# Kernel tuning notes

Hardware: AMD Instinct MI355X
Metric: run time of the kernel (lower is better)

The kernel has to match this reference:

```python
import jax, jax.numpy as jnp
import numpy as np

V, D, H, L, F, S, B = 32000, 1024, 16, 6, 4096, 2048, 2
HD = D // H
EPS = 1e-5


def _pos_encoding(seq_len, d_model):
    pos = jnp.arange(seq_len, dtype=jnp.float32)[:, None]
    div = jnp.exp(jnp.arange(0, d_model, 2, dtype=jnp.float32) * (-np.log(10000.0) / d_model))
    pe = jnp.zeros((seq_len, d_model), dtype=jnp.float32)
    pe = pe.at[:, 0::2].set(jnp.sin(pos * div))
    pe = pe.at[:, 1::2].set(jnp.cos(pos * div))
    return pe


def setup_inputs() -> dict:
    key = jax.random.key(0)
    ks = jax.random.split(key, 16)
    tokens = jax.random.randint(ks[0], (B, S), 0, V, dtype=jnp.int64)
    mask = jnp.ones((B, 1, 1, S), dtype=jnp.int32)
    emb = jax.random.normal(ks[1], (V, D), dtype=jnp.float32) * 0.02
    sa = 1.0 / np.sqrt(D)
    sf = 1.0 / np.sqrt(F)
    return {
        "tokens": tokens,
        "mask": mask,
        "emb": emb,
        "Wq": jax.random.normal(ks[2], (L, D, D), dtype=jnp.float32) * sa,
        "bq": jnp.zeros((L, D), dtype=jnp.float32),
        "Wk": jax.random.normal(ks[3], (L, D, D), dtype=jnp.float32) * sa,
        "bk": jnp.zeros((L, D), dtype=jnp.float32),
        "Wv": jax.random.normal(ks[4], (L, D, D), dtype=jnp.float32) * sa,
        "bv": jnp.zeros((L, D), dtype=jnp.float32),
        "Wo": jax.random.normal(ks[5], (L, D, D), dtype=jnp.float32) * sa,
        "bo": jnp.zeros((L, D), dtype=jnp.float32),
        "W1": jax.random.normal(ks[6], (L, D, F), dtype=jnp.float32) * sa,
        "b1": jnp.zeros((L, F), dtype=jnp.float32),
        "W2": jax.random.normal(ks[7], (L, F, D), dtype=jnp.float32) * sf,
        "b2": jnp.zeros((L, D), dtype=jnp.float32),
        "g1": jnp.ones((L, D), dtype=jnp.float32),
        "be1": jnp.zeros((L, D), dtype=jnp.float32),
        "g2": jnp.ones((L, D), dtype=jnp.float32),
        "be2": jnp.zeros((L, D), dtype=jnp.float32),
    }


def _layer_norm(x, g, b):
    m = jnp.mean(x, axis=-1, keepdims=True)
    v = jnp.mean(jnp.square(x - m), axis=-1, keepdims=True)
    return (x - m) * jax.lax.rsqrt(v + EPS) * g + b


def _encoder_stack(x, mask, params):
    scale = 1.0 / np.sqrt(HD)

    def layer(x, p):
        Wq, bq, Wk, bk, Wv, bv, Wo, bo, W1, b1, W2, b2, g1, be1, g2, be2 = p
        b, s, d = x.shape
        q = (x @ Wq + bq).reshape(b, s, H, HD).transpose(0, 2, 1, 3)  # [B,H,S,HD]
        k = (x @ Wk + bk).reshape(b, s, H, HD).transpose(0, 2, 1, 3)
        v = (x @ Wv + bv).reshape(b, s, H, HD).transpose(0, 2, 1, 3)
        scores = jnp.einsum("bhqd,bhkd->bhqk", q, k) * scale
        scores = jnp.where(mask == 0, -1e9, scores)
        attn = jax.nn.softmax(scores, axis=-1)
        ctx = jnp.einsum("bhqk,bhkd->bhqd", attn, v)
        attn_out = ctx.transpose(0, 2, 1, 3).reshape(b, s, d) @ Wo + bo
        x = _layer_norm(x + attn_out, g1, be1)
        ff = jax.nn.relu(x @ W1 + b1) @ W2 + b2
        x = _layer_norm(x + ff, g2, be2)
        return x, None

    x, _ = jax.lax.scan(layer, x, params)
    return x


def reference(tokens, mask, emb, Wq, bq, Wk, bk, Wv, bv, Wo, bo, W1, b1, W2, b2, g1, be1, g2, be2):
    x = emb[tokens] + _pos_encoding(tokens.shape[1], emb.shape[1])[None]
    params = (Wq, bq, Wk, bk, Wv, bv, Wo, bo, W1, b1, W2, b2, g1, be1, g2, be2)
    return _encoder_stack(x, mask, params)
```

## Files before the change

### kernel.cpp

```cpp
#include <hip/hip_runtime.h>
#include <hip/hip_bf16.h>
#include <cstdint>
#include <cstddef>


typedef __bf16 bf16;
typedef __bf16 bf16x2 __attribute__((ext_vector_type(2)));
typedef __bf16 bf16x4 __attribute__((ext_vector_type(4)));
typedef __bf16 bf16x8 __attribute__((ext_vector_type(8)));
typedef float  f32x4  __attribute__((ext_vector_type(4)));

#define MFMA16(a, b, c) __builtin_amdgcn_mfma_f32_16x16x32_bf16((a), (b), (c), 0, 0, 0)

static __device__ __forceinline__ void load_lds16(const void* g, void* l) {
  __builtin_amdgcn_global_load_lds((const __attribute__((address_space(1))) void*)g,
                                   (__attribute__((address_space(3))) void*)l, 16, 0, 0);
}

#define BAR()   __builtin_amdgcn_s_barrier()
#define SCH0()  __builtin_amdgcn_sched_barrier(0)
#define VMCNT8() asm volatile("s_waitcnt vmcnt(8)" ::: "memory")
#define VMCNT0() asm volatile("s_waitcnt vmcnt(0)" ::: "memory")

__global__ __launch_bounds__(256) void embed_kernel(const int* __restrict__ tok,
                                                    const float* __restrict__ emb,
                                                    bf16* __restrict__ xo) {
  const int row = blockIdx.x;
  const int s = row & 2047;
  const int t = tok[row];
  const int d0 = threadIdx.x * 4;
  const float4 e = *(const float4*)&emb[(size_t)t * 1024 + d0];
  const float* ef = (const float*)&e;
  bf16x4 o4;
#pragma unroll
  for (int j = 0; j < 4; ++j) {
    const int d = d0 + j;
    const float div = __expf(-(float)(d & ~1) * 0.00899447301950864f);
    const float arg = (float)s * div;
    const float pe = (d & 1) ? cosf(arg) : sinf(arg);
    o4[j] = (bf16)(ef[j] + pe);
  }
  *(bf16x4*)&xo[(size_t)row * 1024 + d0] = o4;
}

struct TJob { const float* src; bf16* dst; int K; int N; int t0; };
struct TArgs { TJob j[6]; };

__global__ __launch_bounds__(256) void wtrans_kernel(TArgs a) {
  __shared__ float t[32][33];
  const int blk = blockIdx.x;
  const float* src = a.j[0].src; bf16* dst = a.j[0].dst;
  int K = a.j[0].K, N = a.j[0].N, t0 = a.j[0].t0;
#pragma unroll
  for (int q = 1; q < 6; ++q)
    if (blk >= a.j[q].t0) { src = a.j[q].src; dst = a.j[q].dst; K = a.j[q].K; N = a.j[q].N; t0 = a.j[q].t0; }
  const int tj = blk - t0;
  const int tilesK = K >> 5;
  const int tk = (tj % tilesK) << 5;
  const int tn = (tj / tilesK) << 5;
  const int lx = threadIdx.x & 31, ly = threadIdx.x >> 5;
#pragma unroll
  for (int i = 0; i < 4; ++i)
    t[ly + 8 * i][lx] = src[(size_t)(tk + ly + 8 * i) * N + tn + lx];
  __syncthreads();
#pragma unroll
  for (int i = 0; i < 4; ++i)
    dst[(size_t)(tn + ly + 8 * i) * K + tk + lx] = (bf16)t[lx][ly + 8 * i];
}

__global__ __launch_bounds__(256) void vtrans_kernel(const bf16* __restrict__ v,
                                                     bf16* __restrict__ vt) {
  __shared__ bf16 t[64][72];
  const int bh = blockIdx.y;
  const int s0 = blockIdx.x * 64;
  const int tid = threadIdx.x;
#pragma unroll
  for (int it = 0; it < 2; ++it) {
    const int idx = tid + it * 256;
    const int sr = idx >> 3, h8 = (idx & 7) * 8;
    *(bf16x8*)&t[sr][h8] = *(const bf16x8*)&v[((size_t)bh * 2048 + s0 + sr) * 64 + h8];
  }
  __syncthreads();
#pragma unroll
  for (int it = 0; it < 2; ++it) {
    const int idx = tid + it * 256;
    const int hd = idx >> 3, s8 = (idx & 7) * 8;
    bf16x8 o;
#pragma unroll
    for (int j = 0; j < 8; ++j) o[j] = t[s8 + j][hd];
    *(bf16x8*)&vt[((size_t)bh * 64 + hd) * 2048 + s0 + s8] = o;
  }
}

static __device__ __forceinline__ bf16x8 ldsfrag(const bf16* base, int row, int colb) {
  int off = row * 128 + colb;
  off ^= ((off >> 7) & 7) << 4;
  return *(const bf16x8*)((const char*)base + off);
}

static __device__ __forceinline__ void stage_tile(const bf16* __restrict__ Ag,
    const bf16* __restrict__ Bg, int Kstr, int kt, bf16* lA, bf16* lB, int tid) {
  const char* wbaseA = (const char*)lA + ((tid >> 6) << 10);
  const char* wbaseB = (const char*)lB + ((tid >> 6) << 10);
#pragma unroll
  for (int s = 0; s < 4; ++s) {
    const int L = s * 8192 + tid * 16;
    const int off = L ^ (((L >> 7) & 7) << 4);
    load_lds16(Ag + (size_t)(off >> 7) * Kstr + kt * 64 + ((off & 127) >> 1),
               (void*)(wbaseA + s * 8192));
  }
#pragma unroll
  for (int s = 0; s < 4; ++s) {
    const int L = s * 8192 + tid * 16;
    const int off = L ^ (((L >> 7) & 7) << 4);
    load_lds16(Bg + (size_t)(off >> 7) * Kstr + kt * 64 + ((off & 127) >> 1),
               (void*)(wbaseB + s * 8192));
  }
}

static __device__ __forceinline__ void compute_tile(const bf16* lA, const bf16* lB,
    int wm, int wn, int lr, int lg, f32x4 (&acc)[8][4]) {
  bf16x8 bfr[4][2];
#pragma unroll
  for (int n = 0; n < 4; ++n)
#pragma unroll
    for (int kk = 0; kk < 2; ++kk)
      bfr[n][kk] = ldsfrag(lB, wn * 64 + n * 16 + lr, kk * 64 + lg * 16);
#pragma unroll
  for (int m = 0; m < 8; ++m) {
    const bf16x8 a0 = ldsfrag(lA, wm * 128 + m * 16 + lr, lg * 16);
    const bf16x8 a1 = ldsfrag(lA, wm * 128 + m * 16 + lr, 64 + lg * 16);
    __builtin_amdgcn_s_setprio(1);
#pragma unroll
    for (int n = 0; n < 4; ++n) {
      acc[m][n] = MFMA16(a0, bfr[n][0], acc[m][n]);
      acc[m][n] = MFMA16(a1, bfr[n][1], acc[m][n]);
    }
    __builtin_amdgcn_s_setprio(0);
  }
}

template <int EPI>
__global__ __launch_bounds__(512, 2) void gemm256(
    const bf16* __restrict__ A, const bf16* __restrict__ Bt,
    int Kstr, int Kloop, int Nn, int nbx,
    const float* __restrict__ bias0, const float* __restrict__ bias1,
    const float* __restrict__ bias2, bf16* __restrict__ outb,
    float* __restrict__ pout,
    bf16* __restrict__ q_out, bf16* __restrict__ k_out, bf16* __restrict__ v_out) {
  __shared__ __align__(16) bf16 lds[4][16384];
  const int bz = blockIdx.y;
  const bf16* Abase = A + (size_t)bz * Kloop;
  const bf16* Bbase = Bt + (size_t)bz * Kloop;
  const int cpx = gridDim.x >> 3;
  const int wg = (blockIdx.x & 7) * cpx + (blockIdx.x >> 3);
  const int bx = wg % nbx, by = wg / nbx;
  const int tid = threadIdx.x;
  const int lane = tid & 63, wave = tid >> 6;
  const int lr = lane & 15, lg = lane >> 4;
  const int wm = wave >> 2, wn = wave & 3;
  const int m0 = by * 256, n0 = bx * 256;

  const bf16* Ag = Abase + (size_t)m0 * Kstr;
  const bf16* Bg = Bbase + (size_t)n0 * Kstr;
  bf16* LA0 = lds[0]; bf16* LB0 = lds[1];
  bf16* LA1 = lds[2]; bf16* LB1 = lds[3];

  f32x4 acc[8][4] = {};
  const int T = Kloop >> 6;

  stage_tile(Ag, Bg, Kstr, 0, LA0, LB0, tid);
  stage_tile(Ag, Bg, Kstr, 1, LA1, LB1, tid);
  VMCNT8(); BAR(); SCH0();

  for (int t = 0; t + 3 < T; t += 2) {
    compute_tile(LA0, LB0, wm, wn, lr, lg, acc);
    BAR(); SCH0();
    stage_tile(Ag, Bg, Kstr, t + 2, LA0, LB0, tid);
    VMCNT8(); BAR(); SCH0();
    compute_tile(LA1, LB1, wm, wn, lr, lg, acc);
    BAR(); SCH0();
    stage_tile(Ag, Bg, Kstr, t + 3, LA1, LB1, tid);
    VMCNT8(); BAR(); SCH0();
  }
  compute_tile(LA0, LB0, wm, wn, lr, lg, acc);
  VMCNT0(); BAR(); SCH0();
  compute_tile(LA1, LB1, wm, wn, lr, lg, acc);

#pragma unroll
  for (int m = 0; m < 8; ++m)
#pragma unroll
    for (int n = 0; n < 4; ++n)
#pragma unroll
      for (int r = 0; r < 4; ++r) {
        const int row = m0 + wm * 128 + m * 16 + lg * 4 + r;
        const int col = n0 + wn * 64 + n * 16 + lr;
        float val = acc[m][n][r];
        if (EPI == 0) {
          const int which = col >> 10, hc = col & 1023;
          const float* bs = (which == 0) ? bias0 : (which == 1) ? bias1 : bias2;
          bf16* dst = (which == 0) ? q_out : (which == 1) ? k_out : v_out;
          val += bs[hc];
          const int b = row >> 11, s = row & 2047;
          const int h = hc >> 6, hd = hc & 63;
          dst[(((size_t)b * 16 + h) * 2048 + s) * 64 + hd] = (bf16)val;
        } else if (EPI == 1) {
          pout[(size_t)bz * 4096 * 1024 + (size_t)row * 1024 + col] = val;
        } else {
          val += bias0[col];
          outb[(size_t)row * Nn + col] = (bf16)(val > 0.f ? val : 0.f);
        }
      }
}

__global__ __launch_bounds__(256) void gemm_sk(
    const bf16* __restrict__ A, const bf16* __restrict__ Bt,
    int Kstride, int Kloop, int nbx, float* __restrict__ pout) {
  __shared__ __align__(16) bf16 As[128 * 32];
  __shared__ __align__(16) bf16 Bs[128 * 32];
  const int bz = blockIdx.y;
  const bf16* Ab = A + (size_t)bz * Kloop;
  const bf16* Bb = Bt + (size_t)bz * Kloop;
  float* pb = pout + (size_t)bz * 4096 * 1024;
  const int cpx = gridDim.x >> 3;
  const int wg = (blockIdx.x & 7) * cpx + (blockIdx.x >> 3);
  const int bx = wg % nbx, by = wg / nbx;
  const int tid = threadIdx.x;
  const int lane = tid & 63;
  const int wave = tid >> 6;
  const int lr = lane & 15, lg = lane >> 4;
  const int m0 = by * 128;
  const int n0 = bx * 128;
  const int wr = (wave >> 1) * 64, wc = (wave & 1) * 64;

  f32x4 acc[4][4] = {};

  const int idx0 = tid, idx1 = tid + 256;
  const char* gA0 = (const char*)(Ab + (size_t)(m0 + (idx0 >> 2)) * Kstride) + (idx0 & 3) * 16;
  const char* gA1 = (const char*)(Ab + (size_t)(m0 + (idx1 >> 2)) * Kstride) + (idx1 & 3) * 16;
  const char* gB0 = (const char*)(Bb + (size_t)(n0 + (idx0 >> 2)) * Kstride) + (idx0 & 3) * 16;
  const char* gB1 = (const char*)(Bb + (size_t)(n0 + (idx1 >> 2)) * Kstride) + (idx1 & 3) * 16;
  bf16* lA0 = &As[(wave * 64) * 8];
  bf16* lA1 = &As[(256 + wave * 64) * 8];
  bf16* lB0 = &Bs[(wave * 64) * 8];
  bf16* lB1 = &Bs[(256 + wave * 64) * 8];

  const int ksteps = Kloop >> 5;
  for (int kt = 0; kt < ksteps; ++kt) {
    load_lds16(gA0, lA0); load_lds16(gA1, lA1);
    load_lds16(gB0, lB0); load_lds16(gB1, lB1);
    gA0 += 64; gA1 += 64; gB0 += 64; gB1 += 64;
    __syncthreads();
    bf16x8 af[2], bfr[2];
    bf16x8 af2[2], bfr2[2];
#pragma unroll
    for (int i = 0; i < 4; ++i) {
      bf16x8 a = *(const bf16x8*)&As[(wr + i * 16 + lr) * 32 + lg * 8];
      if (i < 2) af[i] = a; else af2[i - 2] = a;
    }
#pragma unroll
    for (int j = 0; j < 4; ++j) {
      bf16x8 b = *(const bf16x8*)&Bs[(wc + j * 16 + lr) * 32 + lg * 8];
      if (j < 2) bfr[j] = b; else bfr2[j - 2] = b;
    }
#pragma unroll
    for (int i = 0; i < 4; ++i)
#pragma unroll
      for (int j = 0; j < 4; ++j) {
        const bf16x8 a = (i < 2) ? af[i & 1] : af2[i & 1];
        const bf16x8 b = (j < 2) ? bfr[j & 1] : bfr2[j & 1];
        acc[i][j] = MFMA16(a, b, acc[i][j]);
      }
    __syncthreads();
  }

#pragma unroll
  for (int i = 0; i < 4; ++i)
#pragma unroll
    for (int j = 0; j < 4; ++j)
#pragma unroll
      for (int r = 0; r < 4; ++r) {
        const int row = m0 + wr + i * 16 + lg * 4 + r;
        const int col = n0 + wc + j * 16 + lr;
        pb[(size_t)row * 1024 + col] = acc[i][j][r];
      }
}

__global__ __launch_bounds__(256) void attn_kernel(const bf16* __restrict__ q,
                                                   const bf16* __restrict__ k,
                                                   const bf16* __restrict__ vt,
                                                   bf16* __restrict__ ctxo) {
  __shared__ __align__(16) bf16 Kl[64][64];
  __shared__ __align__(16) bf16 Vt[64][64];
  __shared__ __align__(16) bf16 Pl[4][16][64];
  const int tid = threadIdx.x;
  const int lane = tid & 63, w = tid >> 6;
  const int lr = lane & 15, lg = lane >> 4;
  const int swz = lr & 7;
  const int bh = blockIdx.y;
  const int q0 = blockIdx.x * 64;

  const bf16* qp = q + ((size_t)bh * 2048 + q0 + w * 16) * 64;
  bf16x8 qf0 = *(const bf16x8*)&qp[lr * 64 + lg * 8];
  bf16x8 qf1 = *(const bf16x8*)&qp[lr * 64 + lg * 8 + 32];
  const float qs = 0.18033688011112042f;
#pragma unroll
  for (int j = 0; j < 8; ++j) {
    qf0[j] = (bf16)((float)qf0[j] * qs);
    qf1[j] = (bf16)((float)qf1[j] * qs);
  }
  bf16x8 ones8;
#pragma unroll
  for (int j = 0; j < 8; ++j) ones8[j] = (bf16)1.0f;

  const bf16* kbase = k + (size_t)bh * 2048 * 64;
  const bf16* vtb = vt + (size_t)bh * 64 * 2048;

  const int sr0 = tid >> 3, sr1 = sr0 + 32;
  const int c0 = (tid & 7) * 8;
  const int cs0 = c0 ^ ((sr0 & 7) << 3);
  const int cs1 = c0 ^ ((sr1 & 7) << 3);

  f32x4 acc[4] = {};
  f32x4 accl = {};
  float mq = -1e30f;

  bf16x8 kr[2][2], vr[2][2];
  kr[0][0] = *(const bf16x8*)&kbase[(size_t)sr0 * 64 + c0];
  kr[0][1] = *(const bf16x8*)&kbase[(size_t)sr1 * 64 + c0];
  vr[0][0] = *(const bf16x8*)&vtb[(size_t)sr0 * 2048 + c0];
  vr[0][1] = *(const bf16x8*)&vtb[(size_t)sr1 * 2048 + c0];

#pragma unroll 2
  for (int c = 0; c < 32; ++c) {
    const int pp = c & 1;
    *(bf16x8*)&Kl[sr0][cs0] = kr[pp][0];
    *(bf16x8*)&Kl[sr1][cs1] = kr[pp][1];
    *(bf16x8*)&Vt[sr0][cs0] = vr[pp][0];
    *(bf16x8*)&Vt[sr1][cs1] = vr[pp][1];
    if (c + 1 < 32) {
      const int key0n = (c + 1) * 64;
      kr[pp ^ 1][0] = *(const bf16x8*)&kbase[(size_t)(key0n + sr0) * 64 + c0];
      kr[pp ^ 1][1] = *(const bf16x8*)&kbase[(size_t)(key0n + sr1) * 64 + c0];
      vr[pp ^ 1][0] = *(const bf16x8*)&vtb[(size_t)sr0 * 2048 + key0n + c0];
      vr[pp ^ 1][1] = *(const bf16x8*)&vtb[(size_t)sr1 * 2048 + key0n + c0];
    }
    __syncthreads();

    f32x4 st[4];
    __builtin_amdgcn_s_setprio(1);
#pragma unroll
    for (int ks = 0; ks < 4; ++ks) {
      const bf16x8 kf0 = *(const bf16x8*)&Kl[ks * 16 + lr][(lg ^ swz) << 3];
      const bf16x8 kf1 = *(const bf16x8*)&Kl[ks * 16 + lr][((lg + 4) ^ swz) << 3];
      f32x4 sa = {};
      sa = MFMA16(kf0, qf0, sa);
      sa = MFMA16(kf1, qf1, sa);
      st[ks] = sa;
    }
    __builtin_amdgcn_s_setprio(0);

    float mk[4];
#pragma unroll
    for (int ks = 0; ks < 4; ++ks)
      mk[ks] = fmaxf(fmaxf(st[ks][0], st[ks][1]), fmaxf(st[ks][2], st[ks][3]));
    float mx = fmaxf(fmaxf(mk[0], mk[1]), fmaxf(mk[2], mk[3]));
    mx = fmaxf(mx, __shfl_xor(mx, 16));
    mx = fmaxf(mx, __shfl_xor(mx, 32));
    if (!__all(mx - mq <= 8.0f)) {
      const float resc = exp2f(mq - mx);
      mq = mx;
      float rq[4];
#pragma unroll
      for (int r = 0; r < 4; ++r) rq[r] = __shfl(resc, lg * 4 + r);
#pragma unroll
      for (int r = 0; r < 4; ++r) {
        accl[r] *= rq[r];
#pragma unroll
        for (int jn = 0; jn < 4; ++jn) acc[jn][r] *= rq[r];
      }
    }
#pragma unroll
    for (int ks = 0; ks < 4; ++ks) {
      bf16x4 pk;
#pragma unroll
      for (int r = 0; r < 4; ++r) pk[r] = (bf16)exp2f(st[ks][r] - mq);
      const int col = (((ks * 2 + (lg >> 1)) ^ swz) << 3) + ((lg & 1) << 2);
      *(bf16x4*)&Pl[w][lr][col] = pk;
    }

    const bf16x8 pf0 = *(const bf16x8*)&Pl[w][lr][(lg ^ swz) << 3];
    const bf16x8 pf1 = *(const bf16x8*)&Pl[w][lr][((lg + 4) ^ swz) << 3];
    __builtin_amdgcn_s_setprio(1);
#pragma unroll
    for (int jn = 0; jn < 4; ++jn) {
      const bf16x8 vf0 = *(const bf16x8*)&Vt[jn * 16 + lr][(lg ^ swz) << 3];
      const bf16x8 vf1 = *(const bf16x8*)&Vt[jn * 16 + lr][((lg + 4) ^ swz) << 3];
      acc[jn] = MFMA16(pf0, vf0, acc[jn]);
      acc[jn] = MFMA16(pf1, vf1, acc[jn]);
    }
    accl = MFMA16(pf0, ones8, accl);
    accl = MFMA16(pf1, ones8, accl);
    __builtin_amdgcn_s_setprio(0);
    __syncthreads();
  }

  const int bb = bh >> 4, hh = bh & 15;
#pragma unroll
  for (int r = 0; r < 4; ++r) {
    const float inv = 1.f / accl[r];
    const size_t rowg = (size_t)bb * 2048 + q0 + w * 16 + lg * 4 + r;
#pragma unroll
    for (int jn = 0; jn < 4; ++jn)
      ctxo[rowg * 1024 + hh * 64 + jn * 16 + lr] = (bf16)(acc[jn][r] * inv);
  }
}

template <int NP>
__global__ __launch_bounds__(256) void ln2_kernel(const float* __restrict__ p,
                                                  const bf16* __restrict__ resid,
                                                  const float* __restrict__ bias,
                                                  const float* __restrict__ g,
                                                  const float* __restrict__ be,
                                                  bf16* __restrict__ xo) {
  const int row = blockIdx.x, tid = threadIdx.x;
  const bf16x4 rv = *(const bf16x4*)&resid[(size_t)row * 1024 + tid * 4];
  const float4 bb = ((const float4*)bias)[tid];
  float4 v;
  v.x = bb.x + (float)rv[0];
  v.y = bb.y + (float)rv[1];
  v.z = bb.z + (float)rv[2];
  v.w = bb.w + (float)rv[3];
#pragma unroll
  for (int pl = 0; pl < NP; ++pl) {
    const float4 a = ((const float4*)(p + (size_t)pl * 4096 * 1024 + (size_t)row * 1024))[tid];
    v.x += a.x; v.y += a.y; v.z += a.z; v.w += a.w;
  }
  float s = v.x + v.y + v.z + v.w;
  float s2 = v.x * v.x + v.y * v.y + v.z * v.z + v.w * v.w;
#pragma unroll
  for (int o = 32; o > 0; o >>= 1) { s += __shfl_down(s, o); s2 += __shfl_down(s2, o); }
  __shared__ float red[8];
  if ((tid & 63) == 0) { red[tid >> 6] = s; red[4 + (tid >> 6)] = s2; }
  __syncthreads();
  s = red[0] + red[1] + red[2] + red[3];
  s2 = red[4] + red[5] + red[6] + red[7];
  const float mean = s * (1.f / 1024.f);
  const float var = s2 * (1.f / 1024.f) - mean * mean;
  const float rstd = rsqrtf(var + 1e-5f);
  const float4 gv = ((const float4*)g)[tid];
  const float4 bv = ((const float4*)be)[tid];
  bf16x4 o4;
  o4[0] = (bf16)((v.x - mean) * rstd * gv.x + bv.x);
  o4[1] = (bf16)((v.y - mean) * rstd * gv.y + bv.y);
  o4[2] = (bf16)((v.z - mean) * rstd * gv.z + bv.z);
  o4[3] = (bf16)((v.w - mean) * rstd * gv.w + bv.w);
  *(bf16x4*)&xo[(size_t)row * 1024 + tid * 4] = o4;
}

__global__ __launch_bounds__(256) void to_f32_kernel(const bf16* __restrict__ x,
                                                     float* __restrict__ o) {
  const size_t i = ((size_t)blockIdx.x * 256 + threadIdx.x) * 4;
  const bf16x4 v = *(const bf16x4*)&x[i];
  float4 f;
  f.x = (float)v[0]; f.y = (float)v[1]; f.z = (float)v[2]; f.w = (float)v[3];
  *(float4*)&o[i] = f;
}

extern "C" void kernel_launch(void* const* d_in, const int* in_sizes, int n_in,
                              void* d_out, int out_size, void* d_ws, size_t ws_size,
                              hipStream_t stream) {
  const int* tokens = (const int*)d_in[0];
  const float* emb = (const float*)d_in[2];
  const float* Wq = (const float*)d_in[3];
  const float* bq = (const float*)d_in[4];
  const float* Wk = (const float*)d_in[5];
  const float* bk = (const float*)d_in[6];
  const float* Wv = (const float*)d_in[7];
  const float* bv = (const float*)d_in[8];
  const float* Wo = (const float*)d_in[9];
  const float* bo = (const float*)d_in[10];
  const float* W1 = (const float*)d_in[11];
  const float* b1 = (const float*)d_in[12];
  const float* W2 = (const float*)d_in[13];
  const float* b2 = (const float*)d_in[14];
  const float* g1 = (const float*)d_in[15];
  const float* be1 = (const float*)d_in[16];
  const float* g2 = (const float*)d_in[17];
  const float* be2 = (const float*)d_in[18];

  char* p = (char*)d_ws;
  auto carve = [&](size_t bytes) { char* r = p; p += (bytes + 255) & ~(size_t)255; return r; };
  bf16* wt_qkv = (bf16*)carve((size_t)3072 * 1024 * 2);
  bf16* wt_o   = (bf16*)carve((size_t)1024 * 1024 * 2);
  bf16* wt_1   = (bf16*)carve((size_t)4096 * 1024 * 2);
  bf16* wt_2   = (bf16*)carve((size_t)1024 * 4096 * 2);
  bf16* xb     = (bf16*)carve((size_t)4096 * 1024 * 2);
  bf16* qb     = (bf16*)carve((size_t)4096 * 1024 * 2);
  bf16* kb     = (bf16*)carve((size_t)4096 * 1024 * 2);
  bf16* vb     = (bf16*)carve((size_t)4096 * 1024 * 2);
  bf16* vtb    = (bf16*)carve((size_t)4096 * 1024 * 2);
  bf16* ctxb   = (bf16*)carve((size_t)4096 * 1024 * 2);
  float* pb    = (float*)carve((size_t)4 * 4096 * 1024 * 4);
  bf16* hb     = (bf16*)carve((size_t)4096 * 4096 * 2);

  embed_kernel<<<4096, 256, 0, stream>>>(tokens, emb, xb);

  for (int l = 0; l < 6; ++l) {
    TArgs ta;
    ta.j[0] = { Wq + (size_t)l * 1024 * 1024, wt_qkv,                  1024, 1024, 0 };
    ta.j[1] = { Wk + (size_t)l * 1024 * 1024, wt_qkv + 1024 * 1024,    1024, 1024, 1024 };
    ta.j[2] = { Wv + (size_t)l * 1024 * 1024, wt_qkv + 2 * 1024 * 1024,1024, 1024, 2048 };
    ta.j[3] = { Wo + (size_t)l * 1024 * 1024, wt_o,                    1024, 1024, 3072 };
    ta.j[4] = { W1 + (size_t)l * 1024 * 4096, wt_1,                    1024, 4096, 4096 };
    ta.j[5] = { W2 + (size_t)l * 4096 * 1024, wt_2,                    4096, 1024, 8192 };
    wtrans_kernel<<<12288, 256, 0, stream>>>(ta);

    gemm256<0><<<192, 512, 0, stream>>>(xb, wt_qkv, 1024, 1024, 3072, 12,
        bq + (size_t)l * 1024, bk + (size_t)l * 1024, bv + (size_t)l * 1024,
        nullptr, nullptr, qb, kb, vb);

    vtrans_kernel<<<dim3(32, 32), 256, 0, stream>>>(vb, vtb);

    attn_kernel<<<dim3(32, 32), 256, 0, stream>>>(qb, kb, vtb, ctxb);

    gemm_sk<<<dim3(256, 2), 256, 0, stream>>>(ctxb, wt_o, 1024, 512, 8, pb);
    ln2_kernel<2><<<4096, 256, 0, stream>>>(pb, xb, bo + (size_t)l * 1024,
        g1 + (size_t)l * 1024, be1 + (size_t)l * 1024, xb);

    gemm256<2><<<256, 512, 0, stream>>>(xb, wt_1, 1024, 1024, 4096, 16,
        b1 + (size_t)l * 4096, nullptr, nullptr, hb,
        nullptr, nullptr, nullptr, nullptr);

    gemm256<1><<<dim3(64, 4), 512, 0, stream>>>(hb, wt_2, 4096, 1024, 1024, 4,
        nullptr, nullptr, nullptr, nullptr, pb,
        nullptr, nullptr, nullptr);
    ln2_kernel<4><<<4096, 256, 0, stream>>>(pb, xb, b2 + (size_t)l * 1024,
        g2 + (size_t)l * 1024, be2 + (size_t)l * 1024, xb);
  }

  to_f32_kernel<<<4096, 256, 0, stream>>>(xb, (float*)d_out);
}
```

Before: 1.517 ms.

## Double-buffer attention K/V tiles in LDS with direct global-to-LDS loads

Replaces the register-staged K/V prefetch in the attention kernel with global_load_lds transfers into two LDS buffers per operand. Loads for the tile two steps ahead are issued right after the current buffer has been consumed, and vmcnt waits plus barriers keep producer and consumer in step. This is meant to cut the VGPR staging and ds_write instructions and to overlap memory latency with MFMA work. In exchange it doubles the K/V LDS footprint, which may lower occupancy, and it relies on a swizzled source-address computation and manual wait counts being exactly right.

```diff
diff --git a/kernel.cpp b/kernel.cpp
--- a/kernel.cpp
+++ b/kernel.cpp
@@ -20,6 +20,7 @@
 #define BAR()   __builtin_amdgcn_s_barrier()
 #define SCH0()  __builtin_amdgcn_sched_barrier(0)
 #define VMCNT8() asm volatile("s_waitcnt vmcnt(8)" ::: "memory")
+#define VMCNT4() asm volatile("s_waitcnt vmcnt(4)" ::: "memory")
 #define VMCNT0() asm volatile("s_waitcnt vmcnt(0)" ::: "memory")
 
 __global__ __launch_bounds__(256) void embed_kernel(const int* __restrict__ tok,
@@ -290,8 +291,8 @@
                                                    const bf16* __restrict__ k,
                                                    const bf16* __restrict__ vt,
                                                    bf16* __restrict__ ctxo) {
-  __shared__ __align__(16) bf16 Kl[64][64];
-  __shared__ __align__(16) bf16 Vt[64][64];
+  __shared__ __align__(16) bf16 Kl[2][4096];
+  __shared__ __align__(16) bf16 Vl[2][4096];
   __shared__ __align__(16) bf16 Pl[4][16][64];
   const int tid = threadIdx.x;
   const int lane = tid & 63, w = tid >> 6;
@@ -315,44 +316,33 @@
 
   const bf16* kbase = k + (size_t)bh * 2048 * 64;
   const bf16* vtb = vt + (size_t)bh * 64 * 2048;
-
-  const int sr0 = tid >> 3, sr1 = sr0 + 32;
-  const int c0 = (tid & 7) * 8;
-  const int cs0 = c0 ^ ((sr0 & 7) << 3);
-  const int cs1 = c0 ^ ((sr1 & 7) << 3);
+  const int wb = w << 10;
 
   f32x4 acc[4] = {};
   f32x4 accl = {};
   float mq = -1e30f;
 
-  bf16x8 kr[2][2], vr[2][2];
-  kr[0][0] = *(const bf16x8*)&kbase[(size_t)sr0 * 64 + c0];
-  kr[0][1] = *(const bf16x8*)&kbase[(size_t)sr1 * 64 + c0];
-  vr[0][0] = *(const bf16x8*)&vtb[(size_t)sr0 * 2048 + c0];
-  vr[0][1] = *(const bf16x8*)&vtb[(size_t)sr1 * 2048 + c0];
-
-#pragma unroll 2
-  for (int c = 0; c < 32; ++c) {
-    const int pp = c & 1;
-    *(bf16x8*)&Kl[sr0][cs0] = kr[pp][0];
-    *(bf16x8*)&Kl[sr1][cs1] = kr[pp][1];
-    *(bf16x8*)&Vt[sr0][cs0] = vr[pp][0];
-    *(bf16x8*)&Vt[sr1][cs1] = vr[pp][1];
-    if (c + 1 < 32) {
-      const int key0n = (c + 1) * 64;
-      kr[pp ^ 1][0] = *(const bf16x8*)&kbase[(size_t)(key0n + sr0) * 64 + c0];
-      kr[pp ^ 1][1] = *(const bf16x8*)&kbase[(size_t)(key0n + sr1) * 64 + c0];
-      vr[pp ^ 1][0] = *(const bf16x8*)&vtb[(size_t)sr0 * 2048 + key0n + c0];
-      vr[pp ^ 1][1] = *(const bf16x8*)&vtb[(size_t)sr1 * 2048 + key0n + c0];
-    }
-    __syncthreads();
-
+  auto stage = [&](int c, bf16* dK, bf16* dV) {
+    const bf16* gK = kbase + (size_t)c * 64 * 64;
+    const bf16* gV = vtb + c * 64;
+#pragma unroll
+    for (int s = 0; s < 2; ++s) {
+      const int L = s * 4096 + tid * 16;
+      const int off = L ^ (((L >> 7) & 7) << 4);
+      load_lds16(gK + (size_t)(off >> 7) * 64 + ((off & 127) >> 1),
+                 (char*)dK + s * 4096 + wb);
+      load_lds16(gV + (size_t)(off >> 7) * 2048 + ((off & 127) >> 1),
+                 (char*)dV + s * 4096 + wb);
+    }
+  };
+
+  auto body = [&](const bf16* Kb, const bf16* Vb) {
     f32x4 st[4];
     __builtin_amdgcn_s_setprio(1);
 #pragma unroll
     for (int ks = 0; ks < 4; ++ks) {
-      const bf16x8 kf0 = *(const bf16x8*)&Kl[ks * 16 + lr][(lg ^ swz) << 3];
-      const bf16x8 kf1 = *(const bf16x8*)&Kl[ks * 16 + lr][((lg + 4) ^ swz) << 3];
+      const bf16x8 kf0 = *(const bf16x8*)&Kb[(ks * 16 + lr) * 64 + ((lg ^ swz) << 3)];
+      const bf16x8 kf1 = *(const bf16x8*)&Kb[(ks * 16 + lr) * 64 + (((lg + 4) ^ swz) << 3)];
       f32x4 sa = {};
       sa = MFMA16(kf0, qf0, sa);
       sa = MFMA16(kf1, qf1, sa);
@@ -394,16 +384,33 @@
     __builtin_amdgcn_s_setprio(1);
 #pragma unroll
     for (int jn = 0; jn < 4; ++jn) {
-      const bf16x8 vf0 = *(const bf16x8*)&Vt[jn * 16 + lr][(lg ^ swz) << 3];
-      const bf16x8 vf1 = *(const bf16x8*)&Vt[jn * 16 + lr][((lg + 4) ^ swz) << 3];
+      const bf16x8 vf0 = *(const bf16x8*)&Vb[(jn * 16 + lr) * 64 + ((lg ^ swz) << 3)];
+      const bf16x8 vf1 = *(const bf16x8*)&Vb[(jn * 16 + lr) * 64 + (((lg + 4) ^ swz) << 3)];
       acc[jn] = MFMA16(pf0, vf0, acc[jn]);
       acc[jn] = MFMA16(pf1, vf1, acc[jn]);
     }
     accl = MFMA16(pf0, ones8, accl);
     accl = MFMA16(pf1, ones8, accl);
     __builtin_amdgcn_s_setprio(0);
-    __syncthreads();
-  }
+  };
+
+  stage(0, Kl[0], Vl[0]);
+  stage(1, Kl[1], Vl[1]);
+  VMCNT4(); BAR(); SCH0();
+
+  for (int c = 0; c + 3 < 32; c += 2) {
+    body(Kl[0], Vl[0]);
+    BAR(); SCH0();
+    stage(c + 2, Kl[0], Vl[0]);
+    VMCNT4(); BAR(); SCH0();
+    body(Kl[1], Vl[1]);
+    BAR(); SCH0();
+    stage(c + 3, Kl[1], Vl[1]);
+    VMCNT4(); BAR(); SCH0();
+  }
+  body(Kl[0], Vl[0]);
+  VMCNT0(); BAR(); SCH0();
+  body(Kl[1], Vl[1]);
 
   const int bb = bh >> 4, hh = bh & 15;
 #pragma unroll
```

Measured after the change: 1.545 ms. No clear change (+1.8%).
